# Performance work log

Measured on AMD Instinct MI355X. Metric: run time of the kernel, lower is better.

## Reference

```python
import jax, jax.numpy as jnp
import numpy as np

GROUP_SIZE = 128  # QuantizationConfig default


def setup_inputs() -> dict:
    key = jax.random.key(0)
    k0, k1, k2, k3 = jax.random.split(key, 4)
    B, IN, OUT = 32, 4096, 16384
    NG = IN // GROUP_SIZE  # 32 groups
    x = jax.random.normal(k0, (B, IN), dtype=jnp.float16)
    # int8 symmetric-quantized weights in [-127, 127]
    qweight = jax.random.randint(k1, (OUT, IN), -127, 128, dtype=jnp.int8)
    # per-(out_channel, group) fp16 scales; small positive values as produced by absmax/127
    scales = (jax.random.uniform(k2, (OUT, NG), dtype=jnp.float16) * jnp.float16(0.01)
              + jnp.float16(1e-3))
    bias = jax.random.normal(k3, (OUT,), dtype=jnp.float16) * jnp.float16(0.01)
    return {"x": x, "qweight": qweight, "scales": scales, "bias": bias}


def reference(x, qweight, scales, bias):
    # QuantizedLinear._forward_grouped, sym=True, in_features % group_size == 0 path.
    OUT, IN = qweight.shape
    NG = IN // GROUP_SIZE
    # dequantize: [OUT, NG, G] * [OUT, NG, 1] -> [OUT, IN], all in fp16
    w_deq = (qweight.astype(jnp.float16).reshape(OUT, NG, GROUP_SIZE)
             * scales[:, :, None]).reshape(OUT, IN)
    # F.linear(x, w_deq) = x @ w_deq.T, then + bias
    out = jnp.dot(x, w_deq.T) + bias
    return out
```

## Files before the change

kernel.cpp:

```cpp
#include <hip/hip_runtime.h>

typedef __attribute__((ext_vector_type(8))) short short8;
typedef __attribute__((ext_vector_type(4))) float f32x4;
typedef __attribute__((ext_vector_type(4))) int   i32x4;

#define IN_F   4096
#define OUT_F  16384
#define NG     32
#define BK     128
#define NCH    16

static __device__ __forceinline__ short f2bf(float f) {
    union { float f; unsigned u; } c; c.f = f;
    unsigned u = c.u;
    u += 0x7FFF + ((u >> 16) & 1);
    return (short)(u >> 16);
}

static __device__ __forceinline__ short i2bf(int v) {
    union { float f; unsigned u; } c; c.f = (float)v;
    return (short)(c.u >> 16);
}

__global__ __launch_bounds__(256)
void xconv_kernel(const float* __restrict__ x, unsigned short* __restrict__ xT) {
    const int g   = blockIdx.x * 256 + threadIdx.x;
    const int t   = g >> 7;
    const int rem = g & 127;
    const int h   = rem >> 6;
    const int ln  = rem & 63;
    const int l15 = ln >> 2;
    const int l4  = ln & 3;
    const float* src = x + (size_t)(16 * h + l15) * IN_F + t * 32 + l4 * 8;
    f32x4 a = *(const f32x4*)src;
    f32x4 b = *(const f32x4*)(src + 4);
    short8 o;
#pragma unroll
    for (int j = 0; j < 4; ++j) { o[j] = f2bf(a[j]); o[j + 4] = f2bf(b[j]); }
    *(short8*)(xT + (size_t)g * 8) = o;
}

__global__ __launch_bounds__(512, 4)
void qlin_kernel(const unsigned short* __restrict__ xT,
                 const int*   __restrict__ qw,
                 const float* __restrict__ scales,
                 const float* __restrict__ bias,
                 float*       __restrict__ out)
{
    __shared__ int lqw[2][2][32][BK];

    const int tid  = threadIdx.x;
    const int wv   = tid >> 6;
    const int lane = tid & 63;
    const int l15  = lane & 15;
    const int l4   = lane >> 4;
    const int wk   = wv >> 2;
    const int wm   = (wv >> 1) & 1;
    const int wn   = wv & 1;
    const int widx = wv & 3;
    const int col0 = blockIdx.x * 32;

    const int rowB = 16 * wn + l15;
    const int swzB = (rowB & 7) << 4;

    auto STAGE = [&](int c, int sl) {
        const size_t kbase = (size_t)wk * 2048 + (size_t)c * BK;
#pragma unroll
        for (int i = 0; i < 4; ++i) {
            const int p   = widx * 4 + i;
            const int row = 2 * p + (lane >> 5);
            const int byt = ((lane & 31) * 16) ^ ((row & 7) << 4);
            const char* src = (const char*)(qw + (size_t)(col0 + row) * IN_F + kbase) + byt;
            __builtin_amdgcn_global_load_lds(
                (const __attribute__((address_space(1))) unsigned int*)src,
                (__attribute__((address_space(3))) unsigned int*)&lqw[wk][sl][2 * p][0],
                16, 0, 0);
        }
    };

    const unsigned short* xgrp = xT + (size_t)(l15 * 4 + l4) * 8 + (size_t)wm * 512;
    short8 xa[2][4];
    auto XLOAD = [&](int c, int par) {
        const int t = wk * 64 + c * 4;
#pragma unroll
        for (int s = 0; s < 4; ++s)
            xa[par][s] = *(const short8*)(xgrp + (size_t)(t + s) * 1024);
    };

    const float* scr = scales + (size_t)(col0 + rowB) * NG + wk * 16;
    f32x4 sc4[4];
#pragma unroll
    for (int j = 0; j < 4; ++j) sc4[j] = *(const f32x4*)(scr + 4 * j);

    f32x4 acc = {0.f, 0.f, 0.f, 0.f};

    auto COMPUTE = [&](int c, int sl, int par, float sc) {
        const char* lrow = (const char*)&lqw[wk][sl][rowB][0];
        f32x4 ag = {0.f, 0.f, 0.f, 0.f};
#pragma unroll
        for (int s = 0; s < 4; ++s) {
            const int off = (s * 128 + l4 * 32) ^ swzB;
            i32x4 q0 = *(const i32x4*)(lrow + off);
            i32x4 q1 = *(const i32x4*)(lrow + (off ^ 16));
            short8 bfr;
#pragma unroll
            for (int j = 0; j < 4; ++j) { bfr[j] = i2bf(q0[j]); bfr[j + 4] = i2bf(q1[j]); }
            ag = __builtin_amdgcn_mfma_f32_16x16x32_bf16(xa[par][s], bfr, ag, 0, 0, 0);
        }
#pragma unroll
        for (int r = 0; r < 4; ++r) acc[r] += sc * ag[r];
    };

    STAGE(0, 0);
    asm volatile("" ::: "memory");
    XLOAD(0, 0);
    asm volatile("s_waitcnt vmcnt(4)" ::: "memory");
    __builtin_amdgcn_s_barrier();
    __builtin_amdgcn_sched_barrier(0);

#pragma unroll
    for (int i = 0; i <= 14; ++i) {
        STAGE(i + 1, (i + 1) & 1);
        asm volatile("" ::: "memory");
        XLOAD(i + 1, (i + 1) & 1);
        asm volatile("" ::: "memory");
        COMPUTE(i, i & 1, i & 1, sc4[i >> 2][i & 3]);
        asm volatile("s_waitcnt vmcnt(4)" ::: "memory");
        __builtin_amdgcn_s_barrier();
        __builtin_amdgcn_sched_barrier(0);
    }
    COMPUTE(15, 1, 1, sc4[3][3]);

    __syncthreads();
    float* red = (float*)&lqw[0][0][0][0];
    *(f32x4*)&red[(size_t)(wv * 64 + lane) * 4] = acc;
    __syncthreads();
    if (wv < 4) {
        const int col = col0 + rowB;
        const float bv = bias[col];
        f32x4 lo = *(const f32x4*)&red[(size_t)(wv * 64 + lane) * 4];
        f32x4 hi = *(const f32x4*)&red[(size_t)((wv + 4) * 64 + lane) * 4];
#pragma unroll
        for (int r = 0; r < 4; ++r)
            out[(size_t)(16 * wm + l4 * 4 + r) * OUT_F + col] = lo[r] + hi[r] + bv;
    }
}

extern "C" void kernel_launch(void* const* d_in, const int* in_sizes, int n_in,
                              void* d_out, int out_size, void* d_ws, size_t ws_size,
                              hipStream_t stream) {
    const float* x      = (const float*)d_in[0];
    const int*   qw     = (const int*)d_in[1];
    const float* scales = (const float*)d_in[2];
    const float* bias   = (const float*)d_in[3];
    float*       out    = (float*)d_out;
    unsigned short* xT  = (unsigned short*)d_ws;

    hipLaunchKernelGGL(xconv_kernel, dim3(64), dim3(256), 0, stream, x, xT);
    hipLaunchKernelGGL(qlin_kernel, dim3(OUT_F / 32), dim3(512), 0, stream,
                       xT, qw, scales, bias, out);
}
```

Measured before the change: 54.53 us.

## Use triple-buffered LDS pipeline with 64 columns per block

Each block now handles 64 output columns in two sequential 32-column passes, which halves the grid. Each stage loads a 256-wide K slice shared by both K-halves of the waves, and the LDS ring goes from two buffers to three with prefetch distance two. Scales and bias are preloaded into registers. The aim is to hide global-load latency and amortise the prologue and epilogue per block, at the cost of fewer blocks and a lower occupancy hint (2 instead of 4). There is also an extra mid-kernel reduction barrier.

```diff
diff --git a/kernel.cpp b/kernel.cpp
--- a/kernel.cpp
+++ b/kernel.cpp
@@ -7,8 +7,8 @@
 #define IN_F   4096
 #define OUT_F  16384
 #define NG     32
-#define BK     128
-#define NCH    16
+#define BKI    256
+#define NIT    32
 
 static __device__ __forceinline__ short f2bf(float f) {
     union { float f; unsigned u; } c; c.f = f;
@@ -40,14 +40,15 @@
     *(short8*)(xT + (size_t)g * 8) = o;
 }
 
-__global__ __launch_bounds__(512, 4)
+__global__ __launch_bounds__(512, 2)
 void qlin_kernel(const unsigned short* __restrict__ xT,
                  const int*   __restrict__ qw,
                  const float* __restrict__ scales,
                  const float* __restrict__ bias,
                  float*       __restrict__ out)
 {
-    __shared__ int lqw[2][2][32][BK];
+    __shared__ int   lqw[3][32][BKI];
+    __shared__ float red[8][64][4];
 
     const int tid  = threadIdx.x;
     const int wv   = tid >> 6;
@@ -57,93 +58,110 @@
     const int wk   = wv >> 2;
     const int wm   = (wv >> 1) & 1;
     const int wn   = wv & 1;
-    const int widx = wv & 3;
-    const int col0 = blockIdx.x * 32;
-
+    const int colbase = blockIdx.x * 64;
     const int rowB = 16 * wn + l15;
     const int swzB = (rowB & 7) << 4;
 
-    auto STAGE = [&](int c, int sl) {
-        const size_t kbase = (size_t)wk * 2048 + (size_t)c * BK;
+    float sc_arr[NIT];
+    {
+        const float* s0 = scales + (size_t)(colbase + rowB) * NG + wk;
+        const float* s1 = scales + (size_t)(colbase + 32 + rowB) * NG + wk;
+#pragma unroll
+        for (int c = 0; c < 16; ++c) {
+            sc_arr[c]      = s0[2 * c];
+            sc_arr[16 + c] = s1[2 * c];
+        }
+    }
+    const float bv0 = bias[colbase + rowB];
+    const float bv1 = bias[colbase + 32 + rowB];
+
+    auto STAGE = [&](int j, int sl) {
+        const int G = j >> 4, c = j & 15;
+        const int col0 = colbase + G * 32;
 #pragma unroll
         for (int i = 0; i < 4; ++i) {
-            const int p   = widx * 4 + i;
-            const int row = 2 * p + (lane >> 5);
-            const int byt = ((lane & 31) * 16) ^ ((row & 7) << 4);
-            const char* src = (const char*)(qw + (size_t)(col0 + row) * IN_F + kbase) + byt;
+            const int row = 4 * wv + i;
+            const int byt = (lane * 16) ^ ((row & 7) << 4);
+            const char* src = (const char*)(qw + (size_t)(col0 + row) * IN_F + c * BKI) + byt;
             __builtin_amdgcn_global_load_lds(
                 (const __attribute__((address_space(1))) unsigned int*)src,
-                (__attribute__((address_space(3))) unsigned int*)&lqw[wk][sl][2 * p][0],
+                (__attribute__((address_space(3))) unsigned int*)&lqw[sl][row][0],
                 16, 0, 0);
         }
     };
 
     const unsigned short* xgrp = xT + (size_t)(l15 * 4 + l4) * 8 + (size_t)wm * 512;
     short8 xa[2][4];
-    auto XLOAD = [&](int c, int par) {
-        const int t = wk * 64 + c * 4;
+    auto XLOAD = [&](int j, int par) {
+        const int t = (j & 15) * 8 + wk * 4;
 #pragma unroll
         for (int s = 0; s < 4; ++s)
             xa[par][s] = *(const short8*)(xgrp + (size_t)(t + s) * 1024);
     };
 
-    const float* scr = scales + (size_t)(col0 + rowB) * NG + wk * 16;
-    f32x4 sc4[4];
-#pragma unroll
-    for (int j = 0; j < 4; ++j) sc4[j] = *(const f32x4*)(scr + 4 * j);
-
     f32x4 acc = {0.f, 0.f, 0.f, 0.f};
 
-    auto COMPUTE = [&](int c, int sl, int par, float sc) {
-        const char* lrow = (const char*)&lqw[wk][sl][rowB][0];
+    auto COMPUTE = [&](int j, int sl, int par, float sc) {
+        const char* lrow = (const char*)&lqw[sl][rowB][0];
         f32x4 ag = {0.f, 0.f, 0.f, 0.f};
 #pragma unroll
         for (int s = 0; s < 4; ++s) {
-            const int off = (s * 128 + l4 * 32) ^ swzB;
+            const int off = (wk * 512 + s * 128 + l4 * 32) ^ swzB;
             i32x4 q0 = *(const i32x4*)(lrow + off);
             i32x4 q1 = *(const i32x4*)(lrow + (off ^ 16));
             short8 bfr;
 #pragma unroll
-            for (int j = 0; j < 4; ++j) { bfr[j] = i2bf(q0[j]); bfr[j + 4] = i2bf(q1[j]); }
+            for (int u = 0; u < 4; ++u) { bfr[u] = i2bf(q0[u]); bfr[u + 4] = i2bf(q1[u]); }
             ag = __builtin_amdgcn_mfma_f32_16x16x32_bf16(xa[par][s], bfr, ag, 0, 0, 0);
         }
 #pragma unroll
         for (int r = 0; r < 4; ++r) acc[r] += sc * ag[r];
     };
 
+    auto REDSTORE = [&](int G, float bv) {
+        *(f32x4*)&red[wv][lane][0] = acc;
+        asm volatile("s_waitcnt lgkmcnt(0)" ::: "memory");
+        __builtin_amdgcn_s_barrier();
+        if (wv < 4) {
+            const int col = colbase + G * 32 + rowB;
+            f32x4 lo = *(const f32x4*)&red[wv][lane][0];
+            f32x4 hi = *(const f32x4*)&red[wv + 4][lane][0];
+#pragma unroll
+            for (int r = 0; r < 4; ++r)
+                out[(size_t)(16 * wm + l4 * 4 + r) * OUT_F + col] = lo[r] + hi[r] + bv;
+        }
+        acc = (f32x4){0.f, 0.f, 0.f, 0.f};
+    };
+
     STAGE(0, 0);
     asm volatile("" ::: "memory");
     XLOAD(0, 0);
-    asm volatile("s_waitcnt vmcnt(4)" ::: "memory");
+    asm volatile("" ::: "memory");
+    STAGE(1, 1);
+    asm volatile("" ::: "memory");
+    XLOAD(1, 1);
+    asm volatile("s_waitcnt vmcnt(8)" ::: "memory");
     __builtin_amdgcn_s_barrier();
     __builtin_amdgcn_sched_barrier(0);
 
 #pragma unroll
-    for (int i = 0; i <= 14; ++i) {
-        STAGE(i + 1, (i + 1) & 1);
+    for (int j = 0; j < 30; ++j) {
+        COMPUTE(j, j % 3, j & 1, sc_arr[j]);
+        XLOAD(j + 2, j & 1);
         asm volatile("" ::: "memory");
-        XLOAD(i + 1, (i + 1) & 1);
-        asm volatile("" ::: "memory");
-        COMPUTE(i, i & 1, i & 1, sc4[i >> 2][i & 3]);
-        asm volatile("s_waitcnt vmcnt(4)" ::: "memory");
+        STAGE(j + 2, (j + 2) % 3);
+        asm volatile("s_waitcnt vmcnt(8)" ::: "memory");
         __builtin_amdgcn_s_barrier();
         __builtin_amdgcn_sched_barrier(0);
+        if (j == 15) REDSTORE(0, bv0);
     }
-    COMPUTE(15, 1, 1, sc4[3][3]);
 
-    __syncthreads();
-    float* red = (float*)&lqw[0][0][0][0];
-    *(f32x4*)&red[(size_t)(wv * 64 + lane) * 4] = acc;
-    __syncthreads();
-    if (wv < 4) {
-        const int col = col0 + rowB;
-        const float bv = bias[col];
-        f32x4 lo = *(const f32x4*)&red[(size_t)(wv * 64 + lane) * 4];
-        f32x4 hi = *(const f32x4*)&red[(size_t)((wv + 4) * 64 + lane) * 4];
-#pragma unroll
-        for (int r = 0; r < 4; ++r)
-            out[(size_t)(16 * wm + l4 * 4 + r) * OUT_F + col] = lo[r] + hi[r] + bv;
-    }
+    COMPUTE(30, 0, 0, sc_arr[30]);
+    asm volatile("s_waitcnt vmcnt(0)" ::: "memory");
+    __builtin_amdgcn_s_barrier();
+    __builtin_amdgcn_sched_barrier(0);
+    COMPUTE(31, 1, 1, sc_arr[31]);
+    REDSTORE(1, bv1);
 }
 
 extern "C" void kernel_launch(void* const* d_in, const int* in_sizes, int n_in,
@@ -157,6 +175,6 @@
     unsigned short* xT  = (unsigned short*)d_ws;
 
     hipLaunchKernelGGL(xconv_kernel, dim3(64), dim3(256), 0, stream, x, xT);
-    hipLaunchKernelGGL(qlin_kernel, dim3(OUT_F / 32), dim3(512), 0, stream,
+    hipLaunchKernelGGL(qlin_kernel, dim3(OUT_F / 64), dim3(512), 0, stream,
                        xT, qw, scales, bias, out);
 }
```

After: 75.15 us. 37.8% more time.
